# Kernel tuning notes

Hardware: AMD Instinct MI355X
Metric: run time of the kernel (lower is better)

The kernel has to match this reference:

```python
import jax, jax.numpy as jnp
import numpy as np

B, L, D = 2, 4096, 2048
H, K = 32, 16              # num_heads, mini_batch_size
HD = D // H                # head_dim = 64
NMB = L // K               # 256 mini-batches
TTT_BASE_LR = 1.0
LN_EPS = 1e-6


def setup_inputs() -> dict:
    key = jax.random.key(0)
    ks = jax.random.split(key, 16)
    r = lambda k, s: 0.02 * jax.random.normal(k, s, dtype=jnp.float32)
    return {
        "hidden_states": jax.random.normal(ks[0], (B, L, D), dtype=jnp.float32),
        "wq_w": r(ks[1], (D, D)), "wq_b": r(ks[2], (D,)),
        "wk_w": r(ks[3], (D, D)), "wk_b": r(ks[4], (D,)),
        "wv_w": r(ks[5], (D, D)), "wv_b": r(ks[6], (D,)),
        "wo_w": r(ks[7], (D, D)), "wo_b": r(ks[8], (D,)),
        "ttt_norm_weight": 1.0 + r(ks[9], (H, HD)),
        "ttt_norm_bias": r(ks[10], (H, HD)),
        "lr_w": r(ks[11], (H, 1, D)),       # learnable_ttt_lr_weight
        "lr_b": r(ks[12], (H, 1)),          # learnable_ttt_lr_bias
        "W1": r(ks[13], (H, HD, HD)),
        "b1": r(ks[14], (H, 1, HD)),
        "post_norm_w": jnp.ones((D,), jnp.float32),
        "post_norm_b": jnp.zeros((D,), jnp.float32),
    }


def ln_fwd(x, gamma, beta, eps=LN_EPS):
    mu = x.mean(-1, keepdims=True)
    var = ((x - mu) ** 2).mean(-1, keepdims=True)
    return gamma * ((x - mu) / jnp.sqrt(var + eps)) + beta


def ln_fused_l2_bwd(x, l2_target, gamma, beta, eps=LN_EPS):
    # grad of 0.5*||LN(x)*gamma+beta - target||^2 w.r.t. x (standard TTT helper)
    Dd = x.shape[-1]
    mu = x.mean(-1, keepdims=True)
    var = ((x - mu) ** 2).mean(-1, keepdims=True)
    std = jnp.sqrt(var + eps)
    x_hat = (x - mu) / std
    grad_x_hat = (gamma * x_hat + beta - l2_target) * gamma
    return (Dd * grad_x_hat
            - grad_x_hat.sum(-1, keepdims=True)
            - x_hat * (x_hat * grad_x_hat).sum(-1, keepdims=True)) / (Dd * std)


def reference(hidden_states, wq_w, wq_b, wk_w, wk_b, wv_w, wv_b, wo_w, wo_b,
              ttt_norm_weight, ttt_norm_bias, lr_w, lr_b, W1, b1,
              post_norm_w, post_norm_b):
    # QKV projections
    XQ = (hidden_states @ wq_w + wq_b).reshape(B, L, H, HD)
    XK = (hidden_states @ wk_w + wk_b).reshape(B, L, H, HD)
    XV = (hidden_states @ wv_w + wv_b).reshape(B, L, H, HD)
    # L2 normalize q/k per head (F.normalize, eps=1e-12)
    XQ = XQ / jnp.maximum(jnp.linalg.norm(XQ, axis=-1, keepdims=True), 1e-12)
    XK = XK / jnp.maximum(jnp.linalg.norm(XK, axis=-1, keepdims=True), 1e-12)
    # ln_reconstruction_target: torch.std is unbiased (ddof=1), eps added to std
    diff = XV - XK
    mu = diff.mean(-1, keepdims=True)
    std = jnp.std(diff, axis=-1, ddof=1, keepdims=True)
    XV = (ttt_norm_weight[None, None] * ((diff - mu) / (std + 1e-8))
          + ttt_norm_bias[None, None]) + XK
    # reshape to mini-batches: [B,H,NMB,K,HD]
    Xmb = hidden_states.reshape(B, NMB, K, D)
    tohd = lambda t: t.transpose(0, 2, 1, 3).reshape(B, H, NMB, K, HD)
    XQ, XK, XV = tohd(XQ), tohd(XK), tohd(XV)
    # eta gate: einsum('bnkc,hdc->bhnkd') with d==1, sigmoid, scale
    ttt_lr = jnp.einsum('bnkc,hdc->bhnkd', Xmb, lr_w) + lr_b.reshape(1, H, 1, 1, 1)
    ttt_lr = jax.nn.sigmoid(ttt_lr).transpose(0, 1, 2, 4, 3) * (TTT_BASE_LR / HD)  # [B,H,NMB,1,K]
    eta = jnp.broadcast_to(ttt_lr / K, (B, H, NMB, K, K))
    ln_w = ttt_norm_weight[:, None, :]  # [H,1,HD]
    ln_b = ttt_norm_bias[:, None, :]
    tril = jnp.tril(jnp.ones((K, K), jnp.float32))
    W1s = jnp.broadcast_to(W1[None], (B, H, HD, HD))
    b1s = jnp.broadcast_to(b1[None], (B, H, 1, HD))

    def step(carry, xs):
        W1c, b1c = carry
        xq, xk, xv, eta_mb = xs  # [B,H,K,HD], eta [B,H,K,K]
        Z1 = xk @ W1c + b1c
        grad = ln_fused_l2_bwd(Z1, xv - xk, ln_w, ln_b)        # [B,H,K,HD]
        Attn1 = tril * (xq @ xk.transpose(0, 1, 3, 2))         # causal within mini-batch
        b1_bar = b1c - (tril * eta_mb) @ grad
        Z1_bar = xq @ W1c - (eta_mb * Attn1) @ grad + b1_bar
        last_eta = eta_mb[:, :, -1, :, None]                   # [B,H,K,1]
        W1n = W1c - (last_eta * xk).transpose(0, 1, 3, 2) @ grad
        b1n = b1c - jnp.sum(last_eta * grad, axis=-2, keepdims=True)
        out = xq + ln_fwd(Z1_bar, ln_w, ln_b)
        return (W1n, b1n), out

    xs = tuple(t.transpose(2, 0, 1, 3, 4) for t in (XQ, XK, XV, eta))
    _, outs = jax.lax.scan(step, (W1s, b1s), xs)               # [NMB,B,H,K,HD]
    y = outs.transpose(1, 0, 3, 2, 4).reshape(B, L, D)
    # post_norm LayerNorm(eps=1e-6) then output projection
    mu = y.mean(-1, keepdims=True)
    var = ((y - mu) ** 2).mean(-1, keepdims=True)
    y = (y - mu) / jnp.sqrt(var + 1e-6) * post_norm_w + post_norm_b
    return y @ wo_w + wo_b
```

## Files before the change

### kernel.cpp

```cpp
#include <hip/hip_runtime.h>
#include <hip/hip_bf16.h>
#include <cstdint>
#include <cstddef>

#define DEV __device__ __forceinline__

constexpr int Bb = 2, Ls = 4096, Dd = 2048, Hh = 32, HD = 64, MBK = 16, NMBc = 256;
constexpr int MTOK = Bb * Ls;

typedef __bf16 bf16x8 __attribute__((ext_vector_type(8)));
typedef float  f32x4  __attribute__((ext_vector_type(4)));

DEV unsigned short f2bf(float f) {
    union { __bf16 h; unsigned short u; } x;
    x.h = (__bf16)f;
    return x.u;
}
DEV float b2f(unsigned short u) {
    union { unsigned int i; float f; } x; x.i = ((unsigned int)u) << 16;
    return x.f;
}

DEV float wsum64(float v) {
    int t;
    t = __builtin_amdgcn_update_dpp(0, __float_as_int(v), 0x111, 0xf, 0xf, true); v += __int_as_float(t);
    t = __builtin_amdgcn_update_dpp(0, __float_as_int(v), 0x112, 0xf, 0xf, true); v += __int_as_float(t);
    t = __builtin_amdgcn_update_dpp(0, __float_as_int(v), 0x114, 0xf, 0xf, true); v += __int_as_float(t);
    t = __builtin_amdgcn_update_dpp(0, __float_as_int(v), 0x118, 0xf, 0xf, true); v += __int_as_float(t);
    t = __builtin_amdgcn_update_dpp(0, __float_as_int(v), 0x142, 0xa, 0xf, true); v += __int_as_float(t);
    t = __builtin_amdgcn_update_dpp(0, __float_as_int(v), 0x143, 0xc, 0xf, true); v += __int_as_float(t);
    return __int_as_float(__builtin_amdgcn_readlane(__float_as_int(v), 63));
}

DEV float rsum16(float v) {
    int t;
    t = __builtin_amdgcn_update_dpp(0, __float_as_int(v), 0x121, 0xf, 0xf, true); v += __int_as_float(t);
    t = __builtin_amdgcn_update_dpp(0, __float_as_int(v), 0x122, 0xf, 0xf, true); v += __int_as_float(t);
    t = __builtin_amdgcn_update_dpp(0, __float_as_int(v), 0x124, 0xf, 0xf, true); v += __int_as_float(t);
    t = __builtin_amdgcn_update_dpp(0, __float_as_int(v), 0x128, 0xf, 0xf, true); v += __int_as_float(t);
    return v;
}

DEV void g2l16(const void* g, void* l) {
    __builtin_amdgcn_global_load_lds(
        (__attribute__((address_space(1))) void*)(g),
        (__attribute__((address_space(3))) void*)(l), 16, 0, 0);
}

__global__ __launch_bounds__(256) void cast_hs_kernel(const float* __restrict__ src,
                                                      unsigned short* __restrict__ dst) {
    int i = (blockIdx.x * 256 + threadIdx.x) * 4;
    float4 v = *(const float4*)(src + i);
    ushort4 o; o.x = f2bf(v.x); o.y = f2bf(v.y); o.z = f2bf(v.z); o.w = f2bf(v.w);
    *(ushort4*)(dst + i) = o;
}

__global__ __launch_bounds__(256) void transpose_cast_kernel(const float* __restrict__ W,
                                                             unsigned short* __restrict__ Wt) {
    __shared__ float tile[64][65];
    int bx = blockIdx.x & 31;
    int by = blockIdx.x >> 5;
    int t = threadIdx.x;
    int r = t >> 4, c4 = (t & 15) * 4;
    #pragma unroll
    for (int i = 0; i < 4; ++i) {
        int row = r + i * 16;
        float4 v = *(const float4*)(W + (size_t)(bx * 64 + row) * Dd + by * 64 + c4);
        tile[row][c4 + 0] = v.x; tile[row][c4 + 1] = v.y;
        tile[row][c4 + 2] = v.z; tile[row][c4 + 3] = v.w;
    }
    __syncthreads();
    #pragma unroll
    for (int i = 0; i < 4; ++i) {
        int row = r + i * 16;
        ushort4 o;
        o.x = f2bf(tile[c4 + 0][row]); o.y = f2bf(tile[c4 + 1][row]);
        o.z = f2bf(tile[c4 + 2][row]); o.w = f2bf(tile[c4 + 3][row]);
        *(ushort4*)(Wt + (size_t)(by * 64 + row) * Dd + bx * 64 + c4) = o;
    }
}

__global__ __launch_bounds__(256) void gemm_bt_kernel(const unsigned short* __restrict__ A,
                                                      const unsigned short* __restrict__ Bt,
                                                      const float* __restrict__ bias,
                                                      float* __restrict__ C,
                                                      int M, int N, int Kd) {
    __shared__ unsigned short sA[128 * 64];
    __shared__ unsigned short sB[128 * 64];
    int t = threadIdx.x;
    int lane = t & 63;
    int wid = t >> 6, wm = wid >> 1, wn = wid & 1;
    int quad = lane >> 4, c = lane & 15;
    int bm = blockIdx.x, bn = blockIdx.y;

    const unsigned short* pa[4]; const unsigned short* pb[4];
    unsigned short* la[4]; unsigned short* lb[4];
    #pragma unroll
    for (int i = 0; i < 4; ++i) {
        int lin = i * 256 + t;
        int row = lin >> 3, blk = lin & 7;
        int oct = blk ^ (row & 7);
        pa[i] = A  + (size_t)(bm * 128 + row) * Kd + oct * 8;
        pb[i] = Bt + (size_t)(bn * 128 + row) * Kd + oct * 8;
        la[i] = sA + lin * 8;
        lb[i] = sB + lin * 8;
    }

    f32x4 acc[4][4];
    #pragma unroll
    for (int i = 0; i < 4; ++i)
        #pragma unroll
        for (int j = 0; j < 4; ++j)
            #pragma unroll
            for (int r = 0; r < 4; ++r) acc[i][j][r] = 0.f;

    const char* sAc = (const char*)sA;
    const char* sBc = (const char*)sB;
    int rowA0 = wm * 64 + c, rowB0 = wn * 64 + c;
    int sw = (c & 7);

    int nkt = Kd >> 6;
    for (int kt = 0; kt < nkt; ++kt) {
        #pragma unroll
        for (int i = 0; i < 4; ++i) {
            g2l16(pa[i], la[i]);
            g2l16(pb[i], lb[i]);
            pa[i] += 64; pb[i] += 64;
        }
        __syncthreads();
        #pragma unroll
        for (int s = 0; s < 2; ++s) {
            bf16x8 af[4], bfv[4];
            int so = (s << 2) | quad;
            #pragma unroll
            for (int mt = 0; mt < 4; ++mt)
                af[mt] = *(const bf16x8*)(sAc + (rowA0 + mt * 16) * 128 + ((so ^ sw) * 16));
            #pragma unroll
            for (int nt = 0; nt < 4; ++nt)
                bfv[nt] = *(const bf16x8*)(sBc + (rowB0 + nt * 16) * 128 + ((so ^ sw) * 16));
            #pragma unroll
            for (int mt = 0; mt < 4; ++mt)
                #pragma unroll
                for (int nt = 0; nt < 4; ++nt)
                    acc[mt][nt] = __builtin_amdgcn_mfma_f32_16x16x32_bf16(af[mt], bfv[nt], acc[mt][nt], 0, 0, 0);
        }
        __syncthreads();
    }

    float bv[4];
    #pragma unroll
    for (int nt = 0; nt < 4; ++nt) bv[nt] = bias[bn * 128 + wn * 64 + nt * 16 + c];
    #pragma unroll
    for (int mt = 0; mt < 4; ++mt)
        #pragma unroll
        for (int r = 0; r < 4; ++r) {
            int row = bm * 128 + wm * 64 + mt * 16 + quad * 4 + r;
            float* cp = C + (size_t)row * N + bn * 128 + wn * 64 + c;
            #pragma unroll
            for (int nt = 0; nt < 4; ++nt) cp[nt * 16] = acc[mt][nt][r] + bv[nt];
        }
}

__global__ __launch_bounds__(256) void lr_kernel(const float* __restrict__ hs,
                                                 const float* __restrict__ lrw,
                                                 const float* __restrict__ lrb,
                                                 float* __restrict__ lr_out) {
    int tok = blockIdx.x;
    int t = threadIdx.x;
    int h = t >> 3, j0 = t & 7;
    const float* row = hs + (size_t)tok * Dd;
    const float* wr = lrw + (size_t)h * Dd;
    float p = 0.f;
    for (int j = j0 * 4; j < Dd; j += 32) {
        float4 a = *(const float4*)(row + j);
        float4 w = *(const float4*)(wr + j);
        p += a.x * w.x + a.y * w.y + a.z * w.z + a.w * w.w;
    }
    __shared__ float red[32][8];
    red[h][j0] = p;
    __syncthreads();
    if (t < 32) {
        float s = 0.f;
        #pragma unroll
        for (int i = 0; i < 8; ++i) s += red[t][i];
        s += lrb[t];
        s = 1.f / (1.f + expf(-s));
        s *= 1.0f / (HD * MBK);
        int b = tok >> 12, l = tok & (Ls - 1);
        lr_out[(size_t)(b * Hh + t) * Ls + l] = s;
    }
}

DEV void stage_qkv(float4 q, float4 k, float4 v,
                   float* tq, float* tk, float* tv,
                   unsigned short* bq, unsigned short* bk,
                   int rowp, int c4p, float4 lnw4, float4 lnb4) {
    float rq = 1.f / fmaxf(sqrtf(rsum16(q.x*q.x + q.y*q.y + q.z*q.z + q.w*q.w)), 1e-12f);
    q.x *= rq; q.y *= rq; q.z *= rq; q.w *= rq;
    float rk = 1.f / fmaxf(sqrtf(rsum16(k.x*k.x + k.y*k.y + k.z*k.z + k.w*k.w)), 1e-12f);
    k.x *= rk; k.y *= rk; k.z *= rk; k.w *= rk;
    float4 df; df.x = v.x - k.x; df.y = v.y - k.y; df.z = v.z - k.z; df.w = v.w - k.w;
    float mu = rsum16(df.x + df.y + df.z + df.w) * (1.f / 64.f);
    float4 cc; cc.x = df.x - mu; cc.y = df.y - mu; cc.z = df.z - mu; cc.w = df.w - mu;
    float var = rsum16(cc.x*cc.x + cc.y*cc.y + cc.z*cc.z + cc.w*cc.w) * (1.f / 63.f);
    float rs = 1.f / (sqrtf(var) + 1e-8f);
    float4 vn;
    vn.x = lnw4.x * cc.x * rs + lnb4.x + k.x;
    vn.y = lnw4.y * cc.y * rs + lnb4.y + k.y;
    vn.z = lnw4.z * cc.z * rs + lnb4.z + k.z;
    vn.w = lnw4.w * cc.w * rs + lnb4.w + k.w;
    *(float4*)&tq[rowp * 68 + c4p] = q;
    *(float4*)&tk[rowp * 68 + c4p] = k;
    *(float4*)&tv[rowp * 68 + c4p] = vn;
    ushort4 qb, kb;
    qb.x = f2bf(q.x); qb.y = f2bf(q.y); qb.z = f2bf(q.z); qb.w = f2bf(q.w);
    kb.x = f2bf(k.x); kb.y = f2bf(k.y); kb.z = f2bf(k.z); kb.w = f2bf(k.w);
    *(ushort4*)&bq[rowp * 72 + c4p] = qb;
    *(ushort4*)&bk[rowp * 72 + c4p] = kb;
}

__global__ __launch_bounds__(256, 1) void scan_kernel(const float* __restrict__ XQ,
                                                      const float* __restrict__ XK,
                                                      const float* __restrict__ XV,
                                                      const float* __restrict__ lrbuf,
                                                      const float* __restrict__ W1in,
                                                      const float* __restrict__ b1in,
                                                      const float* __restrict__ lnw_g,
                                                      const float* __restrict__ lnb_g,
                                                      float* __restrict__ Y) {
    int bh = blockIdx.x;
    int b = bh >> 5, h = bh & 31;
    int t = threadIdx.x;
    int w = t >> 6;
    int lane = t & 63;
    int q = lane >> 4, n = lane & 15;
    int gc = 16 * w + n;

    __shared__ float tiles[2][3][16 * 68];
    __shared__ unsigned short tbq[2][16 * 72];
    __shared__ unsigned short tbk[2][16 * 72];
    __shared__ float svb[2][16];
    __shared__ unsigned short wt_hi[64 * 72];
    __shared__ unsigned short wt_lo[64 * 72];
    __shared__ float zT[64 * 20];
    __shared__ float zbT[64 * 20];
    __shared__ unsigned short gbufT[64 * 32];
    __shared__ unsigned short sxkT[64 * 32];
    __shared__ unsigned short attb[16 * 32];
    __shared__ float pb[4 * 64];

    #pragma unroll
    for (int i = 0; i < 16; ++i) {
        int k = i * 4 + w;
        float val = W1in[(size_t)h * 4096 + (size_t)k * 64 + lane];
        unsigned short hi = f2bf(val);
        unsigned short lo = f2bf(val - b2f(hi));
        wt_hi[lane * 72 + k] = hi;
        wt_lo[lane * 72 + k] = lo;
    }
    #pragma unroll
    for (int i = 0; i < 8; ++i) { gbufT[i * 256 + t] = 0; sxkT[i * 256 + t] = 0; }
    #pragma unroll
    for (int i = 0; i < 2; ++i) attb[i * 256 + t] = 0;

    float b1r = b1in[h * 64 + lane];
    float lnwr = lnw_g[h * 64 + lane];
    float lnbr = lnb_g[h * 64 + lane];

    const size_t gbase = ((size_t)b * Ls) * Dd + h * 64;
    const float* lrp = lrbuf + (size_t)bh * Ls;

    int rowp = t >> 4, c4p = (t & 15) * 4;
    float4 lnw4 = *(const float4*)(lnw_g + h * 64 + c4p);
    float4 lnb4 = *(const float4*)(lnb_g + h * 64 + c4p);

    {
        float4 q0 = *(const float4*)(XQ + gbase + (size_t)rowp * Dd + c4p);
        float4 k0 = *(const float4*)(XK + gbase + (size_t)rowp * Dd + c4p);
        float4 v0 = *(const float4*)(XV + gbase + (size_t)rowp * Dd + c4p);
        stage_qkv(q0, k0, v0, &tiles[0][0][0], &tiles[0][1][0], &tiles[0][2][0],
                  tbq[0], tbk[0], rowp, c4p, lnw4, lnb4);
    }
    if (t < 16) svb[0][t] = lrp[t];
    float4 preq = *(const float4*)(XQ + gbase + (size_t)(16 + rowp) * Dd + c4p);
    float4 prek = *(const float4*)(XK + gbase + (size_t)(16 + rowp) * Dd + c4p);
    float4 prev = *(const float4*)(XV + gbase + (size_t)(16 + rowp) * Dd + c4p);
    float presv = (t < 16) ? lrp[16 + t] : 0.f;
    __syncthreads();

    const f32x4 zero4 = {0.f, 0.f, 0.f, 0.f};

    for (int nmb = 0; nmb < NMBc; ++nmb) {
        int cb = nmb & 1, nb2 = cb ^ 1;
        int l0 = nmb * 16;
        stage_qkv(preq, prek, prev, &tiles[nb2][0][0], &tiles[nb2][1][0], &tiles[nb2][2][0],
                  tbq[nb2], tbk[nb2], rowp, c4p, lnw4, lnb4);
        if (t < 16) svb[nb2][t] = presv;
        int lp = (l0 + 32 <= Ls - 16) ? (l0 + 32) : (Ls - 16);
        preq = *(const float4*)(XQ + gbase + (size_t)(lp + rowp) * Dd + c4p);
        prek = *(const float4*)(XK + gbase + (size_t)(lp + rowp) * Dd + c4p);
        prev = *(const float4*)(XV + gbase + (size_t)(lp + rowp) * Dd + c4p);
        presv = (t < 16) ? lrp[lp + t] : 0.f;

        const float* xqs = &tiles[cb][0][0];
        const float* xks = &tiles[cb][1][0];
        const float* xvs = &tiles[cb][2][0];
        const unsigned short* bqs = tbq[cb];
        const unsigned short* bks = tbk[cb];

        bf16x8 qf0 = *(const bf16x8*)&bqs[n * 72 + 8 * q];
        bf16x8 qf1 = *(const bf16x8*)&bqs[n * 72 + 32 + 8 * q];
        bf16x8 kf0 = *(const bf16x8*)&bks[n * 72 + 8 * q];
        bf16x8 kf1 = *(const bf16x8*)&bks[n * 72 + 32 + 8 * q];

        bf16x8 wh0 = *(const bf16x8*)&wt_hi[gc * 72 + 8 * q];
        bf16x8 wh1 = *(const bf16x8*)&wt_hi[gc * 72 + 32 + 8 * q];
        bf16x8 wl0 = *(const bf16x8*)&wt_lo[gc * 72 + 8 * q];
        bf16x8 wl1 = *(const bf16x8*)&wt_lo[gc * 72 + 32 + 8 * q];

        f32x4 z1 = __builtin_amdgcn_mfma_f32_16x16x32_bf16(kf0, wh0, zero4, 0, 0, 0);
        z1 = __builtin_amdgcn_mfma_f32_16x16x32_bf16(kf1, wh1, z1, 0, 0, 0);
        f32x4 z1l = __builtin_amdgcn_mfma_f32_16x16x32_bf16(kf0, wl0, zero4, 0, 0, 0);
        z1l = __builtin_amdgcn_mfma_f32_16x16x32_bf16(kf1, wl1, z1l, 0, 0, 0);
        z1 = z1 + z1l;
        f32x4 zb = __builtin_amdgcn_mfma_f32_16x16x32_bf16(qf0, wh0, zero4, 0, 0, 0);
        zb = __builtin_amdgcn_mfma_f32_16x16x32_bf16(qf1, wh1, zb, 0, 0, 0);
        f32x4 zbl = __builtin_amdgcn_mfma_f32_16x16x32_bf16(qf0, wl0, zero4, 0, 0, 0);
        zbl = __builtin_amdgcn_mfma_f32_16x16x32_bf16(qf1, wl1, zbl, 0, 0, 0);
        zb = zb + zbl;

        {
            float4 zs; zs.x = z1[0]; zs.y = z1[1]; zs.z = z1[2]; zs.w = z1[3];
            *(float4*)&zT[gc * 20 + 4 * q] = zs;
        }
        if (w == 0) {
            f32x4 aacc = __builtin_amdgcn_mfma_f32_16x16x32_bf16(qf1, kf1, zero4, 0, 0, 0);
            aacc = __builtin_amdgcn_mfma_f32_16x16x32_bf16(qf0, kf0, aacc, 0, 0, 0);
            float svn = svb[cb][n];
            #pragma unroll
            for (int r = 0; r < 4; ++r) {
                int i = 4 * q + r;
                attb[i * 32 + n] = f2bf((i >= n) ? (-svn * (aacc[r] + 1.f)) : 0.f);
            }
        }
        __syncthreads();

        float4 zz = *(const float4*)&zT[lane * 20 + 4 * w];
        float zar[4] = {zz.x + b1r, zz.y + b1r, zz.z + b1r, zz.w + b1r};
        float xk_rm[4], xv_rm[4], xq_rm[4];
        #pragma unroll
        for (int r = 0; r < 4; ++r) {
            int rw = 4 * w + r;
            xk_rm[r] = xks[rw * 68 + lane];
            xv_rm[r] = xvs[rw * 68 + lane];
            xq_rm[r] = xqs[rw * 68 + lane];
        }
        float4 svr4 = *(const float4*)&svb[cb][4 * w];
        float svr[4] = {svr4.x, svr4.y, svr4.z, svr4.w};
        float gr[4]; float pbv = 0.f;
        #pragma unroll
        for (int r = 0; r < 4; ++r) {
            float s1 = wsum64(zar[r]);
            float s2 = wsum64(zar[r] * zar[r]);
            float mu = s1 * (1.f / 64.f);
            float var = s2 * (1.f / 64.f) - mu * mu;
            float rstd = rsqrtf(var + 1e-6f);
            float xh = (zar[r] - mu) * rstd;
            float g = (lnwr * xh + lnbr - (xv_rm[r] - xk_rm[r])) * lnwr;
            float sg = wsum64(g);
            float sxg = wsum64(xh * g);
            gr[r] = (64.f * g - sg - xh * sxg) * rstd * (1.f / 64.f);
            pbv += svr[r] * gr[r];
        }
        {
            ushort4 gp, sp;
            gp.x = f2bf(gr[0]); gp.y = f2bf(gr[1]); gp.z = f2bf(gr[2]); gp.w = f2bf(gr[3]);
            sp.x = f2bf(svr[0] * xk_rm[0]); sp.y = f2bf(svr[1] * xk_rm[1]);
            sp.z = f2bf(svr[2] * xk_rm[2]); sp.w = f2bf(svr[3] * xk_rm[3]);
            *(ushort4*)&gbufT[lane * 32 + 4 * w] = gp;
            *(ushort4*)&sxkT[lane * 32 + 4 * w] = sp;
            pb[w * 64 + lane] = pbv;
        }
        __syncthreads();

        bf16x8 gF = *(const bf16x8*)&gbufT[gc * 32 + 8 * q];
        bf16x8 amF = *(const bf16x8*)&attb[n * 32 + 8 * q];
        zb = __builtin_amdgcn_mfma_f32_16x16x32_bf16(amF, gF, zb, 0, 0, 0);
        {
            float4 zs; zs.x = zb[0]; zs.y = zb[1]; zs.z = zb[2]; zs.w = zb[3];
            *(float4*)&zbT[gc * 20 + 4 * q] = zs;
        }
        #pragma unroll
        for (int tm = 0; tm < 4; ++tm) {
            bf16x8 ax = *(const bf16x8*)&sxkT[(16 * tm + n) * 32 + 8 * q];
            f32x4 dl = __builtin_amdgcn_mfma_f32_16x16x32_bf16(ax, gF, zero4, 0, 0, 0);
            int ko = 16 * tm + 4 * q;
            ushort4 h4 = *(ushort4*)&wt_hi[gc * 72 + ko];
            ushort4 l4 = *(ushort4*)&wt_lo[gc * 72 + ko];
            float w0 = b2f(h4.x) + b2f(l4.x) - dl[0];
            float w1 = b2f(h4.y) + b2f(l4.y) - dl[1];
            float w2 = b2f(h4.z) + b2f(l4.z) - dl[2];
            float w3 = b2f(h4.w) + b2f(l4.w) - dl[3];
            h4.x = f2bf(w0); l4.x = f2bf(w0 - b2f(h4.x));
            h4.y = f2bf(w1); l4.y = f2bf(w1 - b2f(h4.y));
            h4.z = f2bf(w2); l4.z = f2bf(w2 - b2f(h4.z));
            h4.w = f2bf(w3); l4.w = f2bf(w3 - b2f(h4.w));
            *(ushort4*)&wt_hi[gc * 72 + ko] = h4;
            *(ushort4*)&wt_lo[gc * 72 + ko] = l4;
        }
        float b1n_ = b1r - (pb[0 * 64 + lane] + pb[1 * 64 + lane] +
                            pb[2 * 64 + lane] + pb[3 * 64 + lane]);
        __syncthreads();

        float4 zz2 = *(const float4*)&zbT[lane * 20 + 4 * w];
        float zbr[4] = {zz2.x + b1r, zz2.y + b1r, zz2.z + b1r, zz2.w + b1r};
        #pragma unroll
        for (int r = 0; r < 4; ++r) {
            float s1 = wsum64(zbr[r]);
            float s2 = wsum64(zbr[r] * zbr[r]);
            float mu = s1 * (1.f / 64.f);
            float var = s2 * (1.f / 64.f) - mu * mu;
            float rstd = rsqrtf(var + 1e-6f);
            float o = lnwr * ((zbr[r] - mu) * rstd) + lnbr + xq_rm[r];
            Y[gbase + (size_t)(l0 + 4 * w + r) * Dd + lane] = o;
        }
        b1r = b1n_;
    }
}

__global__ __launch_bounds__(256) void postnorm_kernel(const float* __restrict__ Y,
                                                       const float* __restrict__ pw,
                                                       const float* __restrict__ pb,
                                                       unsigned short* __restrict__ Yb) {
    int tok = blockIdx.x, t = threadIdx.x;
    const float* row = Y + (size_t)tok * Dd;
    int c0 = t * 4, c1 = 1024 + t * 4;
    float4 v0 = *(const float4*)(row + c0);
    float4 v1 = *(const float4*)(row + c1);
    float s1 = v0.x + v0.y + v0.z + v0.w + v1.x + v1.y + v1.z + v1.w;
    float s2 = v0.x * v0.x + v0.y * v0.y + v0.z * v0.z + v0.w * v0.w +
               v1.x * v1.x + v1.y * v1.y + v1.z * v1.z + v1.w * v1.w;
    s1 = wsum64(s1); s2 = wsum64(s2);
    __shared__ float r1[4], r2[4];
    if ((t & 63) == 0) { r1[t >> 6] = s1; r2[t >> 6] = s2; }
    __syncthreads();
    float S1 = r1[0] + r1[1] + r1[2] + r1[3];
    float S2 = r2[0] + r2[1] + r2[2] + r2[3];
    float mu = S1 * (1.f / 2048.f);
    float var = S2 * (1.f / 2048.f) - mu * mu;
    float rstd = rsqrtf(var + 1e-6f);
    float4 w0 = *(const float4*)(pw + c0), b0 = *(const float4*)(pb + c0);
    float4 w1 = *(const float4*)(pw + c1), b1 = *(const float4*)(pb + c1);
    ushort4 o0, o1;
    o0.x = f2bf((v0.x - mu) * rstd * w0.x + b0.x);
    o0.y = f2bf((v0.y - mu) * rstd * w0.y + b0.y);
    o0.z = f2bf((v0.z - mu) * rstd * w0.z + b0.z);
    o0.w = f2bf((v0.w - mu) * rstd * w0.w + b0.w);
    o1.x = f2bf((v1.x - mu) * rstd * w1.x + b1.x);
    o1.y = f2bf((v1.y - mu) * rstd * w1.y + b1.y);
    o1.z = f2bf((v1.z - mu) * rstd * w1.z + b1.z);
    o1.w = f2bf((v1.w - mu) * rstd * w1.w + b1.w);
    *(ushort4*)(Yb + (size_t)tok * Dd + c0) = o0;
    *(ushort4*)(Yb + (size_t)tok * Dd + c1) = o1;
}

extern "C" void kernel_launch(void* const* d_in, const int* in_sizes, int n_in,
                              void* d_out, int out_size, void* d_ws, size_t ws_size,
                              hipStream_t stream) {
    const float* hs   = (const float*)d_in[0];
    const float* wq_w = (const float*)d_in[1];
    const float* wq_b = (const float*)d_in[2];
    const float* wk_w = (const float*)d_in[3];
    const float* wk_b = (const float*)d_in[4];
    const float* wv_w = (const float*)d_in[5];
    const float* wv_b = (const float*)d_in[6];
    const float* wo_w = (const float*)d_in[7];
    const float* wo_b = (const float*)d_in[8];
    const float* lnw  = (const float*)d_in[9];
    const float* lnb  = (const float*)d_in[10];
    const float* lr_w = (const float*)d_in[11];
    const float* lr_b = (const float*)d_in[12];
    const float* W1   = (const float*)d_in[13];
    const float* b1   = (const float*)d_in[14];
    const float* pnw  = (const float*)d_in[15];
    const float* pnb  = (const float*)d_in[16];
    float* out = (float*)d_out;

    char* ws = (char*)d_ws;
    size_t off = 0;
    auto alloc = [&](size_t bytes) -> void* {
        void* p = ws + off; off += (bytes + 255) & ~(size_t)255; return p;
    };
    unsigned short* hsb = (unsigned short*)alloc((size_t)MTOK * Dd * 2);
    unsigned short* wtb = (unsigned short*)alloc((size_t)Dd * Dd * 2);
    float* XQ = (float*)alloc((size_t)MTOK * Dd * 4);
    float* XK = (float*)alloc((size_t)MTOK * Dd * 4);
    float* XV = (float*)alloc((size_t)MTOK * Dd * 4);
    float* lrbuf = (float*)alloc((size_t)Bb * Hh * Ls * 4);
    float* Y = XQ;
    unsigned short* Yb = hsb;

    dim3 blk(256);
    cast_hs_kernel<<<dim3(MTOK * Dd / 1024), blk, 0, stream>>>(hs, hsb);

    transpose_cast_kernel<<<dim3(1024), blk, 0, stream>>>(wq_w, wtb);
    gemm_bt_kernel<<<dim3(64, 16), blk, 0, stream>>>(hsb, wtb, wq_b, XQ, MTOK, Dd, Dd);
    transpose_cast_kernel<<<dim3(1024), blk, 0, stream>>>(wk_w, wtb);
    gemm_bt_kernel<<<dim3(64, 16), blk, 0, stream>>>(hsb, wtb, wk_b, XK, MTOK, Dd, Dd);
    transpose_cast_kernel<<<dim3(1024), blk, 0, stream>>>(wv_w, wtb);
    gemm_bt_kernel<<<dim3(64, 16), blk, 0, stream>>>(hsb, wtb, wv_b, XV, MTOK, Dd, Dd);

    lr_kernel<<<dim3(MTOK), blk, 0, stream>>>(hs, lr_w, lr_b, lrbuf);

    scan_kernel<<<dim3(Bb * Hh), blk, 0, stream>>>(XQ, XK, XV, lrbuf, W1, b1, lnw, lnb, Y);

    postnorm_kernel<<<dim3(MTOK), blk, 0, stream>>>(Y, pnw, pnb, Yb);

    transpose_cast_kernel<<<dim3(1024), blk, 0, stream>>>(wo_w, wtb);
    gemm_bt_kernel<<<dim3(64, 16), blk, 0, stream>>>(Yb, wtb, wo_b, out, MTOK, Dd, Dd);
}
```

Measured before the change: 1.413 ms.

## Precompute masked attention tiles in parallel kernel and cut cross-lane reductions in scan

Adds an attn_kernel that computes the eta-scaled causal q·k attention matrix for every mini-batch in parallel and writes it as bf16 into a reused workspace. The sequential scan then prefetches that tile instead of computing it on wave 0 each step. The scan also replaces the transpose-through-LDS plus 64-lane wavefront reductions for both layer norms with 16-lane row partial sums combined through small shared arrays, and writes outputs in the MFMA column layout. The aim is to shorten the serial per-step critical path, at the cost of an extra kernel launch and extra global traffic.

```diff
diff --git a/kernel.cpp b/kernel.cpp
--- a/kernel.cpp
+++ b/kernel.cpp
@@ -38,6 +38,20 @@
     t = __builtin_amdgcn_update_dpp(0, __float_as_int(v), 0x122, 0xf, 0xf, true); v += __int_as_float(t);
     t = __builtin_amdgcn_update_dpp(0, __float_as_int(v), 0x124, 0xf, 0xf, true); v += __int_as_float(t);
     t = __builtin_amdgcn_update_dpp(0, __float_as_int(v), 0x128, 0xf, 0xf, true); v += __int_as_float(t);
+    return v;
+}
+
+DEV float qsum4(float v) {
+    int t;
+    t = __builtin_amdgcn_update_dpp(0, __float_as_int(v), 0xB1, 0xf, 0xf, true); v += __int_as_float(t);
+    t = __builtin_amdgcn_update_dpp(0, __float_as_int(v), 0x4E, 0xf, 0xf, true); v += __int_as_float(t);
+    return v;
+}
+
+DEV float sel4(int n, float a, float b, float c, float d) {
+    float v = (n == 1) ? b : a;
+    v = (n == 2) ? c : v;
+    v = (n == 3) ? d : v;
     return v;
 }
 
@@ -188,6 +202,62 @@
         s *= 1.0f / (HD * MBK);
         int b = tok >> 12, l = tok & (Ls - 1);
         lr_out[(size_t)(b * Hh + t) * Ls + l] = s;
+    }
+}
+
+__global__ __launch_bounds__(256) void attn_kernel(const float* __restrict__ XQ,
+                                                   const float* __restrict__ XK,
+                                                   const float* __restrict__ lrbuf,
+                                                   unsigned short* __restrict__ attG) {
+    __shared__ unsigned short qb[4][16 * 72];
+    __shared__ unsigned short kb[4][16 * 72];
+    int t = threadIdx.x, w = t >> 6, lane = t & 63;
+    int gid = blockIdx.x * 4 + w;
+    int bh = gid >> 8, nmb = gid & 255;
+    int b = bh >> 5, h = bh & 31;
+    int l0 = nmb * 16;
+    int tok = lane >> 2, fq = lane & 3;
+    size_t base = ((size_t)(b * Ls) + l0 + tok) * Dd + h * 64 + fq * 16;
+    float4 qv[4], kv[4];
+    #pragma unroll
+    for (int i = 0; i < 4; ++i) {
+        qv[i] = *(const float4*)(XQ + base + 4 * i);
+        kv[i] = *(const float4*)(XK + base + 4 * i);
+    }
+    float sq = 0.f, sk = 0.f;
+    #pragma unroll
+    for (int i = 0; i < 4; ++i) {
+        sq += qv[i].x * qv[i].x + qv[i].y * qv[i].y + qv[i].z * qv[i].z + qv[i].w * qv[i].w;
+        sk += kv[i].x * kv[i].x + kv[i].y * kv[i].y + kv[i].z * kv[i].z + kv[i].w * kv[i].w;
+    }
+    float rq = 1.f / fmaxf(sqrtf(qsum4(sq)), 1e-12f);
+    float rk = 1.f / fmaxf(sqrtf(qsum4(sk)), 1e-12f);
+    #pragma unroll
+    for (int i = 0; i < 4; ++i) {
+        ushort4 oq, ok;
+        oq.x = f2bf(qv[i].x * rq); oq.y = f2bf(qv[i].y * rq);
+        oq.z = f2bf(qv[i].z * rq); oq.w = f2bf(qv[i].w * rq);
+        ok.x = f2bf(kv[i].x * rk); ok.y = f2bf(kv[i].y * rk);
+        ok.z = f2bf(kv[i].z * rk); ok.w = f2bf(kv[i].w * rk);
+        *(ushort4*)&qb[w][tok * 72 + fq * 16 + 4 * i] = oq;
+        *(ushort4*)&kb[w][tok * 72 + fq * 16 + 4 * i] = ok;
+    }
+    __syncthreads();
+    int q2 = lane >> 4, n = lane & 15;
+    bf16x8 qf0 = *(const bf16x8*)&qb[w][n * 72 + 8 * q2];
+    bf16x8 qf1 = *(const bf16x8*)&qb[w][n * 72 + 32 + 8 * q2];
+    bf16x8 kf0 = *(const bf16x8*)&kb[w][n * 72 + 8 * q2];
+    bf16x8 kf1 = *(const bf16x8*)&kb[w][n * 72 + 32 + 8 * q2];
+    const f32x4 zero4 = {0.f, 0.f, 0.f, 0.f};
+    f32x4 a = __builtin_amdgcn_mfma_f32_16x16x32_bf16(qf1, kf1, zero4, 0, 0, 0);
+    a = __builtin_amdgcn_mfma_f32_16x16x32_bf16(qf0, kf0, a, 0, 0, 0);
+    float svn = lrbuf[(size_t)bh * Ls + l0 + n];
+    unsigned short* op = attG + ((size_t)bh * NMBc + nmb) * 256;
+    #pragma unroll
+    for (int r = 0; r < 4; ++r) {
+        int i = 4 * q2 + r;
+        float v = (i >= n) ? (-svn * (a[r] + 1.f)) : 0.f;
+        op[i * 16 + n] = f2bf(v);
     }
 }
 
@@ -223,6 +293,7 @@
                                                       const float* __restrict__ XK,
                                                       const float* __restrict__ XV,
                                                       const float* __restrict__ lrbuf,
+                                                      const unsigned short* __restrict__ attG,
                                                       const float* __restrict__ W1in,
                                                       const float* __restrict__ b1in,
                                                       const float* __restrict__ lnw_g,
@@ -242,12 +313,13 @@
     __shared__ float svb[2][16];
     __shared__ unsigned short wt_hi[64 * 72];
     __shared__ unsigned short wt_lo[64 * 72];
-    __shared__ float zT[64 * 20];
-    __shared__ float zbT[64 * 20];
+    __shared__ float zTr[16 * 68];
     __shared__ unsigned short gbufT[64 * 32];
     __shared__ unsigned short sxkT[64 * 32];
     __shared__ unsigned short attb[16 * 32];
     __shared__ float pb[4 * 64];
+    __shared__ float s1p[16 * 4], s2p[16 * 4];
+    __shared__ float s1z[16 * 4], s2z[16 * 4];
 
     #pragma unroll
     for (int i = 0; i < 16; ++i) {
@@ -264,11 +336,16 @@
     for (int i = 0; i < 2; ++i) attb[i * 256 + t] = 0;
 
     float b1r = b1in[h * 64 + lane];
+    float b1c = b1in[h * 64 + gc];
     float lnwr = lnw_g[h * 64 + lane];
     float lnbr = lnb_g[h * 64 + lane];
+    float lnwc = lnw_g[h * 64 + gc];
+    float lnbc = lnb_g[h * 64 + gc];
 
     const size_t gbase = ((size_t)b * Ls) * Dd + h * 64;
     const float* lrp = lrbuf + (size_t)bh * Ls;
+    const unsigned short* attp_base = attG + (size_t)bh * NMBc * 256;
+    int arow = 4 * w + (lane >> 2), ac4 = (lane & 3) * 4;
 
     int rowp = t >> 4, c4p = (t & 15) * 4;
     float4 lnw4 = *(const float4*)(lnw_g + h * 64 + c4p);
@@ -286,6 +363,8 @@
     float4 prek = *(const float4*)(XK + gbase + (size_t)(16 + rowp) * Dd + c4p);
     float4 prev = *(const float4*)(XV + gbase + (size_t)(16 + rowp) * Dd + c4p);
     float presv = (t < 16) ? lrp[16 + t] : 0.f;
+    ushort4 attp = {0, 0, 0, 0};
+    if (lane < 16) attp = *(const ushort4*)(attp_base + arow * 16 + ac4);
     __syncthreads();
 
     const f32x4 zero4 = {0.f, 0.f, 0.f, 0.f};
@@ -296,6 +375,11 @@
         stage_qkv(preq, prek, prev, &tiles[nb2][0][0], &tiles[nb2][1][0], &tiles[nb2][2][0],
                   tbq[nb2], tbk[nb2], rowp, c4p, lnw4, lnb4);
         if (t < 16) svb[nb2][t] = presv;
+        if (lane < 16) {
+            *(ushort4*)&attb[arow * 32 + ac4] = attp;
+            int ap = (nmb + 1 < NMBc) ? (nmb + 1) : (NMBc - 1);
+            attp = *(const ushort4*)(attp_base + (size_t)ap * 256 + arow * 16 + ac4);
+        }
         int lp = (l0 + 32 <= Ls - 16) ? (l0 + 32) : (Ls - 16);
         preq = *(const float4*)(XQ + gbase + (size_t)(lp + rowp) * Dd + c4p);
         prek = *(const float4*)(XK + gbase + (size_t)(lp + rowp) * Dd + c4p);
@@ -329,39 +413,41 @@
         zbl = __builtin_amdgcn_mfma_f32_16x16x32_bf16(qf1, wl1, zbl, 0, 0, 0);
         zb = zb + zbl;
 
+        #pragma unroll
+        for (int r = 0; r < 4; ++r) zTr[(4 * q + r) * 68 + gc] = z1[r];
         {
-            float4 zs; zs.x = z1[0]; zs.y = z1[1]; zs.z = z1[2]; zs.w = z1[3];
-            *(float4*)&zT[gc * 20 + 4 * q] = zs;
-        }
-        if (w == 0) {
-            f32x4 aacc = __builtin_amdgcn_mfma_f32_16x16x32_bf16(qf1, kf1, zero4, 0, 0, 0);
-            aacc = __builtin_amdgcn_mfma_f32_16x16x32_bf16(qf0, kf0, aacc, 0, 0, 0);
-            float svn = svb[cb][n];
+            float p1[4], p2[4];
             #pragma unroll
             for (int r = 0; r < 4; ++r) {
-                int i = 4 * q + r;
-                attb[i * 32 + n] = f2bf((i >= n) ? (-svn * (aacc[r] + 1.f)) : 0.f);
+                float za = z1[r] + b1c;
+                p1[r] = rsum16(za);
+                p2[r] = rsum16(za * za);
             }
+            if (n < 4) {
+                s1p[(4 * q + n) * 4 + w] = sel4(n, p1[0], p1[1], p1[2], p1[3]);
+                s2p[(4 * q + n) * 4 + w] = sel4(n, p2[0], p2[1], p2[2], p2[3]);
+            }
         }
         __syncthreads();
 
-        float4 zz = *(const float4*)&zT[lane * 20 + 4 * w];
-        float zar[4] = {zz.x + b1r, zz.y + b1r, zz.z + b1r, zz.w + b1r};
-        float xk_rm[4], xv_rm[4], xq_rm[4];
+        float xk_rm[4], xv_rm[4], zar[4];
         #pragma unroll
         for (int r = 0; r < 4; ++r) {
             int rw = 4 * w + r;
+            zar[r] = zTr[rw * 68 + lane] + b1r;
             xk_rm[r] = xks[rw * 68 + lane];
             xv_rm[r] = xvs[rw * 68 + lane];
-            xq_rm[r] = xqs[rw * 68 + lane];
         }
         float4 svr4 = *(const float4*)&svb[cb][4 * w];
         float svr[4] = {svr4.x, svr4.y, svr4.z, svr4.w};
         float gr[4]; float pbv = 0.f;
         #pragma unroll
         for (int r = 0; r < 4; ++r) {
-            float s1 = wsum64(zar[r]);
-            float s2 = wsum64(zar[r] * zar[r]);
+            int rw = 4 * w + r;
+            float4 a1 = *(const float4*)&s1p[rw * 4];
+            float4 a2 = *(const float4*)&s2p[rw * 4];
+            float s1 = a1.x + a1.y + a1.z + a1.w;
+            float s2 = a2.x + a2.y + a2.z + a2.w;
             float mu = s1 * (1.f / 64.f);
             float var = s2 * (1.f / 64.f) - mu * mu;
             float rstd = rsqrtf(var + 1e-6f);
@@ -386,9 +472,20 @@
         bf16x8 gF = *(const bf16x8*)&gbufT[gc * 32 + 8 * q];
         bf16x8 amF = *(const bf16x8*)&attb[n * 32 + 8 * q];
         zb = __builtin_amdgcn_mfma_f32_16x16x32_bf16(amF, gF, zb, 0, 0, 0);
+        float zbar[4], xqc[4];
         {
-            float4 zs; zs.x = zb[0]; zs.y = zb[1]; zs.z = zb[2]; zs.w = zb[3];
-            *(float4*)&zbT[gc * 20 + 4 * q] = zs;
+            float pz1[4], pz2[4];
+            #pragma unroll
+            for (int r = 0; r < 4; ++r) {
+                zbar[r] = zb[r] + b1c;
+                pz1[r] = rsum16(zbar[r]);
+                pz2[r] = rsum16(zbar[r] * zbar[r]);
+                xqc[r] = xqs[(4 * q + r) * 68 + gc];
+            }
+            if (n < 4) {
+                s1z[(4 * q + n) * 4 + w] = sel4(n, pz1[0], pz1[1], pz1[2], pz1[3]);
+                s2z[(4 * q + n) * 4 + w] = sel4(n, pz2[0], pz2[1], pz2[2], pz2[3]);
+            }
         }
         #pragma unroll
         for (int tm = 0; tm < 4; ++tm) {
@@ -408,23 +505,26 @@
             *(ushort4*)&wt_hi[gc * 72 + ko] = h4;
             *(ushort4*)&wt_lo[gc * 72 + ko] = l4;
         }
-        float b1n_ = b1r - (pb[0 * 64 + lane] + pb[1 * 64 + lane] +
-                            pb[2 * 64 + lane] + pb[3 * 64 + lane]);
+        float b1r_n = b1r - (pb[0 * 64 + lane] + pb[64 + lane] +
+                             pb[128 + lane] + pb[192 + lane]);
+        float b1c_n = b1c - (pb[0 * 64 + gc] + pb[64 + gc] +
+                             pb[128 + gc] + pb[192 + gc]);
         __syncthreads();
 
-        float4 zz2 = *(const float4*)&zbT[lane * 20 + 4 * w];
-        float zbr[4] = {zz2.x + b1r, zz2.y + b1r, zz2.z + b1r, zz2.w + b1r};
         #pragma unroll
         for (int r = 0; r < 4; ++r) {
-            float s1 = wsum64(zbr[r]);
-            float s2 = wsum64(zbr[r] * zbr[r]);
+            int row = 4 * q + r;
+            float4 a1 = *(const float4*)&s1z[row * 4];
+            float4 a2 = *(const float4*)&s2z[row * 4];
+            float s1 = a1.x + a1.y + a1.z + a1.w;
+            float s2 = a2.x + a2.y + a2.z + a2.w;
             float mu = s1 * (1.f / 64.f);
             float var = s2 * (1.f / 64.f) - mu * mu;
             float rstd = rsqrtf(var + 1e-6f);
-            float o = lnwr * ((zbr[r] - mu) * rstd) + lnbr + xq_rm[r];
-            Y[gbase + (size_t)(l0 + 4 * w + r) * Dd + lane] = o;
-        }
-        b1r = b1n_;
+            float o = lnwc * ((zbar[r] - mu) * rstd) + lnbc + xqc[r];
+            Y[gbase + (size_t)(l0 + row) * Dd + gc] = o;
+        }
+        b1r = b1r_n; b1c = b1c_n;
     }
 }
 
@@ -499,6 +599,7 @@
     float* lrbuf = (float*)alloc((size_t)Bb * Hh * Ls * 4);
     float* Y = XQ;
     unsigned short* Yb = hsb;
+    unsigned short* attG = hsb;
 
     dim3 blk(256);
     cast_hs_kernel<<<dim3(MTOK * Dd / 1024), blk, 0, stream>>>(hs, hsb);
@@ -511,8 +612,9 @@
     gemm_bt_kernel<<<dim3(64, 16), blk, 0, stream>>>(hsb, wtb, wv_b, XV, MTOK, Dd, Dd);
 
     lr_kernel<<<dim3(MTOK), blk, 0, stream>>>(hs, lr_w, lr_b, lrbuf);
-
-    scan_kernel<<<dim3(Bb * Hh), blk, 0, stream>>>(XQ, XK, XV, lrbuf, W1, b1, lnw, lnb, Y);
+    attn_kernel<<<dim3(Bb * Hh * NMBc / 4), blk, 0, stream>>>(XQ, XK, lrbuf, attG);
+
+    scan_kernel<<<dim3(Bb * Hh), blk, 0, stream>>>(XQ, XK, XV, lrbuf, attG, W1, b1, lnw, lnb, Y);
 
     postnorm_kernel<<<dim3(MTOK), blk, 0, stream>>>(Y, pnw, pnb, Yb);
 
```

Result: slower. 1.448 ms (+2.4%).
